# Kernel tuning notes

Measured on AMD Instinct MI355X. Metric: run time of the kernel, lower is better.

## Reference

```python
import jax, jax.numpy as jnp
import numpy as np

N_NODES = 50000
N_EDGES = 800000
IN_F = 128
OUT_F = 128
EDGE_F = 6


def setup_inputs() -> dict:
    key = jax.random.key(0)
    k1, k2, k3, k4, k5, k6, k7 = jax.random.split(key, 7)
    nodeFeatures = jax.random.normal(k1, (N_NODES, IN_F), dtype=jnp.float32)
    edgeIndex = jax.random.randint(k2, (N_EDGES, 2), 0, N_NODES, dtype=jnp.int64)
    edgeFeatures = jax.random.normal(k3, (N_EDGES, EDGE_F), dtype=jnp.float32)
    # nn.Linear params (kaiming-uniform-ish init scale)
    lim_n = 1.0 / np.sqrt(IN_F)
    lim_e = 1.0 / np.sqrt(EDGE_F)
    W = jax.random.uniform(k4, (IN_F, OUT_F), minval=-lim_n, maxval=lim_n, dtype=jnp.float32)
    b = jax.random.uniform(k5, (OUT_F,), minval=-lim_n, maxval=lim_n, dtype=jnp.float32)
    We = jax.random.uniform(k6, (EDGE_F, OUT_F), minval=-lim_e, maxval=lim_e, dtype=jnp.float32)
    be = jax.random.uniform(k7, (OUT_F,), minval=-lim_e, maxval=lim_e, dtype=jnp.float32)
    return {"nodeFeatures": nodeFeatures, "edgeIndex": edgeIndex,
            "edgeFeatures": edgeFeatures, "W": W, "b": b, "We": We, "be": be}


def reference(nodeFeatures, edgeIndex, edgeFeatures, W, b, We, be):
    # node linear: [N, out]
    transformed = nodeFeatures @ W + b
    # edge linear: [E, out]
    edgeMsg = edgeFeatures @ We + be
    src = edgeIndex[:, 0]
    dst = edgeIndex[:, 1]
    # per-edge message = transformed[src] + edgeMsg, scatter-add into dst
    messages = transformed[src] + edgeMsg  # [E, out]
    aggregated = jax.ops.segment_sum(messages, dst, num_segments=nodeFeatures.shape[0])
    return jax.nn.relu(aggregated)
```

## Files before the change

### kernel.cpp

```cpp
#include <hip/hip_runtime.h>
#include <hip/hip_bf16.h>
#include <stdint.h>

#define IN_F 128
#define EDGE_F 6

using bf16x8 = __attribute__((ext_vector_type(8))) short;
using f32x4  = __attribute__((ext_vector_type(4))) float;

__device__ __forceinline__ float bf2f(unsigned short u) {
    return __uint_as_float(((unsigned int)u) << 16);
}
__device__ __forceinline__ unsigned short f2bfbits(float f) {
    __hip_bfloat16 h = __float2bfloat16(f);
    return *reinterpret_cast<unsigned short*>(&h);
}
__device__ __forceinline__ unsigned int packbf(float a, float b) {
    return ((unsigned int)f2bfbits(b) << 16) | (unsigned int)f2bfbits(a);
}

__global__ __launch_bounds__(256) void hist_cast(
        const int* __restrict__ eidx, const float* __restrict__ ef,
        int* __restrict__ cnt, int* __restrict__ rank,
        uint4* __restrict__ efp, int n_edges,
        const float* __restrict__ nf, unsigned short* __restrict__ nfb,
        int n_cast) {
    const int t = blockIdx.x * 256 + threadIdx.x;
    if (t < n_edges) {
        const int2 pr = reinterpret_cast<const int2*>(eidx)[t];
        const float2* efs = reinterpret_cast<const float2*>(ef + (size_t)t * EDGE_F);
        const float2 f0 = efs[0], f1 = efs[1], f2 = efs[2];
        uint4 q;
        q.x = (unsigned int)pr.x;
        q.y = packbf(f0.x, f0.y);
        q.z = packbf(f1.x, f1.y);
        q.w = packbf(f2.x, f2.y);
        efp[t] = q;
        rank[t] = atomicAdd(&cnt[pr.y], 1);
    }
    const int stride = gridDim.x * 256;
    for (int i = t; i < n_cast; i += stride) {
        const float4 lo = reinterpret_cast<const float4*>(nf)[2 * i];
        const float4 hi = reinterpret_cast<const float4*>(nf)[2 * i + 1];
        uint4 o;
        o.x = packbf(lo.x, lo.y); o.y = packbf(lo.z, lo.w);
        o.z = packbf(hi.x, hi.y); o.w = packbf(hi.z, hi.w);
        reinterpret_cast<uint4*>(nfb)[i] = o;
    }
}

__global__ __launch_bounds__(256) void scan_fused(
        const int* __restrict__ cnt, int* __restrict__ rowptr, int n, int nblk,
        unsigned long long* __restrict__ agg,
        const float* __restrict__ W, const float* __restrict__ b,
        const float* __restrict__ We, const float* __restrict__ be,
        unsigned short* __restrict__ Wpack, float* __restrict__ W2pack) {
    const int tid = threadIdx.x;
    const int blk = blockIdx.x;
    if (blk == nblk) {
        for (int idx = tid; idx < 16384; idx += 256) {
            int j = idx & 7, lane = (idx >> 3) & 63, ft = (idx >> 9) & 7, kb = idx >> 12;
            int k = kb * 32 + (lane >> 4) * 8 + j;
            int f = ft * 16 + (lane & 15);
            Wpack[idx] = f2bfbits(W[k * 128 + f]);
        }
        for (int idx = tid; idx < 1024; idx += 256) {
            int j = idx >> 7, f = idx & 127;
            float w = 0.f;
            if (j < 6)       w = We[j * 128 + f];
            else if (j == 6) w = b[f] + be[f];
            W2pack[idx] = w;
        }
        return;
    }
    __shared__ int sh[256];
    const int idx = blk * 256 + tid;
    const int v = (idx < n) ? cnt[idx] : 0;
    sh[tid] = v;
    __syncthreads();
    for (int off = 1; off < 256; off <<= 1) {
        int t2 = (tid >= off) ? sh[tid - off] : 0;
        __syncthreads();
        sh[tid] += t2;
        __syncthreads();
    }
    const int incl = sh[tid];
    if (tid == 0)
        atomicExch(&agg[blk], (1ULL << 32) | (unsigned int)sh[255]);
    int pre = 0;
    if (tid < blk) {
        unsigned long long x;
        do { x = atomicAdd(&agg[tid], 0ULL); } while ((x >> 32) == 0);
        pre = (int)(unsigned int)x;
    }
    __syncthreads();
    sh[tid] = pre;
    __syncthreads();
    for (int off = 128; off > 0; off >>= 1) {
        if (tid < off) sh[tid] += sh[tid + off];
        __syncthreads();
    }
    const int off0 = sh[0];
    if (idx < n) rowptr[idx] = off0 + incl - v;
    if (blk == nblk - 1 && tid == 255) rowptr[n] = off0 + incl;
}

__global__ __launch_bounds__(256) void fill_csr(
        const int* __restrict__ eidx, const int* __restrict__ rowptr,
        const int* __restrict__ rank, const uint4* __restrict__ efp,
        uint4* __restrict__ rec, int n_edges) {
    int e = blockIdx.x * 256 + threadIdx.x;
    if (e >= n_edges) return;
    const int dst = reinterpret_cast<const int2*>(eidx)[e].y;
    const int pos = rowptr[dst] + rank[e];
    rec[pos] = efp[e];
}

__global__ __launch_bounds__(256) void aggregate_bf16(
        const unsigned short* __restrict__ nfb, const uint4* __restrict__ rec,
        const int* __restrict__ rowptr, unsigned short* __restrict__ S,
        unsigned short* __restrict__ E8, int n_nodes) {
    const int lane = threadIdx.x & 63;
    const int wv = __builtin_amdgcn_readfirstlane(threadIdx.x >> 6);
    const int n = blockIdx.x * 4 + wv;
    if (n >= n_nodes) return;
    const int r0 = rowptr[n], r1 = rowptr[n + 1];
    const int deg = r1 - r0;
    float ax = 0.f, ay = 0.f;
    float e0 = 0.f, e1 = 0.f, e2 = 0.f, e3 = 0.f, e4 = 0.f, e5 = 0.f;
    int i = r0;
    for (; i + 7 < r1; i += 8) {
        uint4 q[8];
        unsigned int u[8];
#pragma unroll
        for (int j = 0; j < 8; ++j) q[j] = rec[i + j];
#pragma unroll
        for (int j = 0; j < 8; ++j)
            u[j] = reinterpret_cast<const unsigned int*>(nfb + (size_t)(int)q[j].x * IN_F)[lane];
#pragma unroll
        for (int j = 0; j < 8; ++j) {
            ax += bf2f((unsigned short)u[j]);
            ay += bf2f((unsigned short)(u[j] >> 16));
            e0 += bf2f((unsigned short)q[j].y);
            e1 += bf2f((unsigned short)(q[j].y >> 16));
            e2 += bf2f((unsigned short)q[j].z);
            e3 += bf2f((unsigned short)(q[j].z >> 16));
            e4 += bf2f((unsigned short)q[j].w);
            e5 += bf2f((unsigned short)(q[j].w >> 16));
        }
    }
    for (; i + 3 < r1; i += 4) {
        uint4 q[4];
        unsigned int u[4];
#pragma unroll
        for (int j = 0; j < 4; ++j) q[j] = rec[i + j];
#pragma unroll
        for (int j = 0; j < 4; ++j)
            u[j] = reinterpret_cast<const unsigned int*>(nfb + (size_t)(int)q[j].x * IN_F)[lane];
#pragma unroll
        for (int j = 0; j < 4; ++j) {
            ax += bf2f((unsigned short)u[j]);
            ay += bf2f((unsigned short)(u[j] >> 16));
            e0 += bf2f((unsigned short)q[j].y);
            e1 += bf2f((unsigned short)(q[j].y >> 16));
            e2 += bf2f((unsigned short)q[j].z);
            e3 += bf2f((unsigned short)(q[j].z >> 16));
            e4 += bf2f((unsigned short)q[j].w);
            e5 += bf2f((unsigned short)(q[j].w >> 16));
        }
    }
    for (; i < r1; ++i) {
        const uint4 q0 = rec[i];
        const unsigned int u0 = reinterpret_cast<const unsigned int*>(nfb + (size_t)(int)q0.x * IN_F)[lane];
        ax += bf2f((unsigned short)u0); ay += bf2f((unsigned short)(u0 >> 16));
        e0 += bf2f((unsigned short)q0.y); e1 += bf2f((unsigned short)(q0.y >> 16));
        e2 += bf2f((unsigned short)q0.z); e3 += bf2f((unsigned short)(q0.z >> 16));
        e4 += bf2f((unsigned short)q0.w); e5 += bf2f((unsigned short)(q0.w >> 16));
    }
    unsigned short* row = S + (size_t)n * IN_F;
    reinterpret_cast<unsigned int*>(row)[lane] = packbf(ax, ay);
    if (lane == 0) {
        uint4 q;
        q.x = packbf(e0, e1);
        q.y = packbf(e2, e3);
        q.z = packbf(e4, e5);
        q.w = packbf((float)deg, 0.f);
        *reinterpret_cast<uint4*>(E8 + (size_t)n * 8) = q;
    }
}

__global__ __launch_bounds__(256) void gemm_mfma(
        const unsigned short* __restrict__ S, const unsigned short* __restrict__ E8,
        const unsigned short* __restrict__ Wpack, const float* __restrict__ W2pack,
        float* __restrict__ out, int n_nodes) {
    __shared__ __align__(16) short Wl[16384];
    __shared__ float W2l[1024];
    const int tid = threadIdx.x;
    for (int i = tid; i < 2048; i += 256)
        reinterpret_cast<uint4*>(Wl)[i] = reinterpret_cast<const uint4*>(Wpack)[i];
    for (int i = tid; i < 1024; i += 256) W2l[i] = W2pack[i];

    const int wv = tid >> 6, lane = tid & 63;
    const int m = lane & 15, quad = lane >> 4;
    const int n0 = blockIdx.x * 64 + wv * 16;

    const int arow = min(n0 + m, n_nodes - 1);
    const unsigned short* ap = S + (size_t)arow * IN_F + quad * 8;
    bf16x8 a[4];
#pragma unroll
    for (int kb = 0; kb < 4; ++kb)
        a[kb] = *reinterpret_cast<const bf16x8*>(ap + kb * 32);

    __syncthreads();

    f32x4 acc[8];
#pragma unroll
    for (int ft = 0; ft < 8; ++ft) acc[ft] = (f32x4){0.f, 0.f, 0.f, 0.f};

#pragma unroll
    for (int kb = 0; kb < 4; ++kb) {
#pragma unroll
        for (int ft = 0; ft < 8; ++ft) {
            const bf16x8 bfrag =
                reinterpret_cast<const bf16x8*>(Wl)[(kb * 8 + ft) * 64 + lane];
            acc[ft] = __builtin_amdgcn_mfma_f32_16x16x32_bf16(a[kb], bfrag, acc[ft], 0, 0, 0);
        }
    }

    float e[4][7];
#pragma unroll
    for (int r = 0; r < 4; ++r) {
        const int n = min(n0 + quad * 4 + r, n_nodes - 1);
        const uint4 q = *reinterpret_cast<const uint4*>(E8 + (size_t)n * 8);
        e[r][0] = bf2f((unsigned short)q.x); e[r][1] = bf2f((unsigned short)(q.x >> 16));
        e[r][2] = bf2f((unsigned short)q.y); e[r][3] = bf2f((unsigned short)(q.y >> 16));
        e[r][4] = bf2f((unsigned short)q.z); e[r][5] = bf2f((unsigned short)(q.z >> 16));
        e[r][6] = bf2f((unsigned short)q.w);
    }
#pragma unroll
    for (int ft = 0; ft < 8; ++ft) {
        const int f = ft * 16 + m;
        float w2[7];
#pragma unroll
        for (int j = 0; j < 7; ++j) w2[j] = W2l[j * 128 + f];
#pragma unroll
        for (int r = 0; r < 4; ++r) {
            const int n = n0 + quad * 4 + r;
            if (n < n_nodes) {
                float v = acc[ft][r];
#pragma unroll
                for (int j = 0; j < 7; ++j) v += e[r][j] * w2[j];
                out[(size_t)n * 128 + f] = fmaxf(v, 0.f);
            }
        }
    }
}

extern "C" void kernel_launch(void* const* d_in, const int* in_sizes, int n_in,
                              void* d_out, int out_size, void* d_ws, size_t ws_size,
                              hipStream_t stream) {
    const float* nf = (const float*)d_in[0];
    const int* eidx = (const int*)d_in[1];
    const float* ef = (const float*)d_in[2];
    const float* W  = (const float*)d_in[3];
    const float* b  = (const float*)d_in[4];
    const float* We = (const float*)d_in[5];
    const float* be = (const float*)d_in[6];
    float* out = (float*)d_out;

    const int n_nodes = in_sizes[0] / IN_F;
    const int n_edges = in_sizes[1] / 2;

    uint4* rec = (uint4*)d_ws;
    uint4* efp = rec + n_edges;
    unsigned short* S = (unsigned short*)(efp + n_edges);
    unsigned short* E8 = S + (size_t)n_nodes * IN_F;
    unsigned short* Wpack = E8 + (size_t)n_nodes * 8;
    float* W2pack = (float*)(Wpack + 16384);
    int* cnt = (int*)(W2pack + 1024);
    unsigned long long* agg = (unsigned long long*)(cnt + n_nodes);
    int* rowptr = (int*)(agg + 256);
    int* rank   = rowptr + n_nodes + 1;
    unsigned short* nfb = (unsigned short*)(rank + n_edges);

    hipMemsetAsync(cnt, 0, (size_t)n_nodes * 4 + 256 * 8, stream);

    const int eb = (n_edges + 255) / 256;
    const int nblk = (n_nodes + 255) / 256;
    const int n_cast = n_nodes * (IN_F / 8);

    hist_cast<<<eb, 256, 0, stream>>>(eidx, ef, cnt, rank, efp, n_edges, nf, nfb, n_cast);
    scan_fused<<<nblk + 1, 256, 0, stream>>>(cnt, rowptr, n_nodes, nblk, agg,
                                             W, b, We, be, Wpack, W2pack);
    fill_csr<<<eb, 256, 0, stream>>>(eidx, rowptr, rank, efp, rec, n_edges);

    aggregate_bf16<<<(n_nodes + 3) / 4, 256, 0, stream>>>(nfb, rec, rowptr, S, E8, n_nodes);
    gemm_mfma<<<(n_nodes + 63) / 64, 256, 0, stream>>>(S, E8, Wpack, W2pack, out, n_nodes);
}
```

Before: 206.8 us.

## Fuse neighbor aggregation and MFMA GEMM into one kernel via LDS staging

Merges the aggregation kernel and the GEMM kernel. Each 256-thread block aggregates 64 destination rows into padded shared memory, then runs the MFMA projection straight from LDS. W fragments are read from global/L2 instead of being staged in shared memory. This removes the S/E8 global round trip and one kernel launch. In exchange, only 782 blocks remain, each wave serially gathers 16 rows, and the MFMA phase waits on the slowest row, so latency hiding and load balance may get worse.

```diff
diff --git a/kernel.cpp b/kernel.cpp
--- a/kernel.cpp
+++ b/kernel.cpp
@@ -4,6 +4,8 @@
 
 #define IN_F 128
 #define EDGE_F 6
+#define ROWS 64
+#define RSTRIDE 136
 
 using bf16x8 = __attribute__((ext_vector_type(8))) short;
 using f32x4  = __attribute__((ext_vector_type(4))) float;
@@ -116,103 +118,97 @@
     rec[pos] = efp[e];
 }
 
-__global__ __launch_bounds__(256) void aggregate_bf16(
+__global__ __launch_bounds__(256) void agg_gemm(
         const unsigned short* __restrict__ nfb, const uint4* __restrict__ rec,
-        const int* __restrict__ rowptr, unsigned short* __restrict__ S,
-        unsigned short* __restrict__ E8, int n_nodes) {
-    const int lane = threadIdx.x & 63;
-    const int wv = __builtin_amdgcn_readfirstlane(threadIdx.x >> 6);
-    const int n = blockIdx.x * 4 + wv;
-    if (n >= n_nodes) return;
-    const int r0 = rowptr[n], r1 = rowptr[n + 1];
-    const int deg = r1 - r0;
-    float ax = 0.f, ay = 0.f;
-    float e0 = 0.f, e1 = 0.f, e2 = 0.f, e3 = 0.f, e4 = 0.f, e5 = 0.f;
-    int i = r0;
-    for (; i + 7 < r1; i += 8) {
-        uint4 q[8];
-        unsigned int u[8];
-#pragma unroll
-        for (int j = 0; j < 8; ++j) q[j] = rec[i + j];
-#pragma unroll
-        for (int j = 0; j < 8; ++j)
-            u[j] = reinterpret_cast<const unsigned int*>(nfb + (size_t)(int)q[j].x * IN_F)[lane];
-#pragma unroll
-        for (int j = 0; j < 8; ++j) {
-            ax += bf2f((unsigned short)u[j]);
-            ay += bf2f((unsigned short)(u[j] >> 16));
-            e0 += bf2f((unsigned short)q[j].y);
-            e1 += bf2f((unsigned short)(q[j].y >> 16));
-            e2 += bf2f((unsigned short)q[j].z);
-            e3 += bf2f((unsigned short)(q[j].z >> 16));
-            e4 += bf2f((unsigned short)q[j].w);
-            e5 += bf2f((unsigned short)(q[j].w >> 16));
-        }
-    }
-    for (; i + 3 < r1; i += 4) {
-        uint4 q[4];
-        unsigned int u[4];
-#pragma unroll
-        for (int j = 0; j < 4; ++j) q[j] = rec[i + j];
-#pragma unroll
-        for (int j = 0; j < 4; ++j)
-            u[j] = reinterpret_cast<const unsigned int*>(nfb + (size_t)(int)q[j].x * IN_F)[lane];
-#pragma unroll
-        for (int j = 0; j < 4; ++j) {
-            ax += bf2f((unsigned short)u[j]);
-            ay += bf2f((unsigned short)(u[j] >> 16));
-            e0 += bf2f((unsigned short)q[j].y);
-            e1 += bf2f((unsigned short)(q[j].y >> 16));
-            e2 += bf2f((unsigned short)q[j].z);
-            e3 += bf2f((unsigned short)(q[j].z >> 16));
-            e4 += bf2f((unsigned short)q[j].w);
-            e5 += bf2f((unsigned short)(q[j].w >> 16));
-        }
-    }
-    for (; i < r1; ++i) {
-        const uint4 q0 = rec[i];
-        const unsigned int u0 = reinterpret_cast<const unsigned int*>(nfb + (size_t)(int)q0.x * IN_F)[lane];
-        ax += bf2f((unsigned short)u0); ay += bf2f((unsigned short)(u0 >> 16));
-        e0 += bf2f((unsigned short)q0.y); e1 += bf2f((unsigned short)(q0.y >> 16));
-        e2 += bf2f((unsigned short)q0.z); e3 += bf2f((unsigned short)(q0.z >> 16));
-        e4 += bf2f((unsigned short)q0.w); e5 += bf2f((unsigned short)(q0.w >> 16));
-    }
-    unsigned short* row = S + (size_t)n * IN_F;
-    reinterpret_cast<unsigned int*>(row)[lane] = packbf(ax, ay);
-    if (lane == 0) {
-        uint4 q;
-        q.x = packbf(e0, e1);
-        q.y = packbf(e2, e3);
-        q.z = packbf(e4, e5);
-        q.w = packbf((float)deg, 0.f);
-        *reinterpret_cast<uint4*>(E8 + (size_t)n * 8) = q;
-    }
-}
-
-__global__ __launch_bounds__(256) void gemm_mfma(
-        const unsigned short* __restrict__ S, const unsigned short* __restrict__ E8,
+        const int* __restrict__ rowptr,
         const unsigned short* __restrict__ Wpack, const float* __restrict__ W2pack,
         float* __restrict__ out, int n_nodes) {
-    __shared__ __align__(16) short Wl[16384];
-    __shared__ float W2l[1024];
+    __shared__ __align__(16) unsigned short Sl[ROWS * RSTRIDE];
+    __shared__ __align__(16) unsigned short E8l[ROWS * 8];
     const int tid = threadIdx.x;
-    for (int i = tid; i < 2048; i += 256)
-        reinterpret_cast<uint4*>(Wl)[i] = reinterpret_cast<const uint4*>(Wpack)[i];
-    for (int i = tid; i < 1024; i += 256) W2l[i] = W2pack[i];
-
-    const int wv = tid >> 6, lane = tid & 63;
+    const int lane = tid & 63;
+    const int wv = tid >> 6;
+    const int nb0 = blockIdx.x * ROWS;
+
+    for (int r = wv; r < ROWS; r += 4) {
+        const int n = nb0 + r;
+        float ax = 0.f, ay = 0.f;
+        float e0 = 0.f, e1 = 0.f, e2 = 0.f, e3 = 0.f, e4 = 0.f, e5 = 0.f;
+        int deg = 0;
+        if (n < n_nodes) {
+            const int r0 = rowptr[n], r1 = rowptr[n + 1];
+            deg = r1 - r0;
+            int i = r0;
+            for (; i + 7 < r1; i += 8) {
+                uint4 q[8];
+                unsigned int u[8];
+#pragma unroll
+                for (int j = 0; j < 8; ++j) q[j] = rec[i + j];
+#pragma unroll
+                for (int j = 0; j < 8; ++j)
+                    u[j] = reinterpret_cast<const unsigned int*>(nfb + (size_t)(int)q[j].x * IN_F)[lane];
+#pragma unroll
+                for (int j = 0; j < 8; ++j) {
+                    ax += bf2f((unsigned short)u[j]);
+                    ay += bf2f((unsigned short)(u[j] >> 16));
+                    e0 += bf2f((unsigned short)q[j].y);
+                    e1 += bf2f((unsigned short)(q[j].y >> 16));
+                    e2 += bf2f((unsigned short)q[j].z);
+                    e3 += bf2f((unsigned short)(q[j].z >> 16));
+                    e4 += bf2f((unsigned short)q[j].w);
+                    e5 += bf2f((unsigned short)(q[j].w >> 16));
+                }
+            }
+            for (; i + 3 < r1; i += 4) {
+                uint4 q[4];
+                unsigned int u[4];
+#pragma unroll
+                for (int j = 0; j < 4; ++j) q[j] = rec[i + j];
+#pragma unroll
+                for (int j = 0; j < 4; ++j)
+                    u[j] = reinterpret_cast<const unsigned int*>(nfb + (size_t)(int)q[j].x * IN_F)[lane];
+#pragma unroll
+                for (int j = 0; j < 4; ++j) {
+                    ax += bf2f((unsigned short)u[j]);
+                    ay += bf2f((unsigned short)(u[j] >> 16));
+                    e0 += bf2f((unsigned short)q[j].y);
+                    e1 += bf2f((unsigned short)(q[j].y >> 16));
+                    e2 += bf2f((unsigned short)q[j].z);
+                    e3 += bf2f((unsigned short)(q[j].z >> 16));
+                    e4 += bf2f((unsigned short)q[j].w);
+                    e5 += bf2f((unsigned short)(q[j].w >> 16));
+                }
+            }
+            for (; i < r1; ++i) {
+                const uint4 q0 = rec[i];
+                const unsigned int u0 = reinterpret_cast<const unsigned int*>(nfb + (size_t)(int)q0.x * IN_F)[lane];
+                ax += bf2f((unsigned short)u0); ay += bf2f((unsigned short)(u0 >> 16));
+                e0 += bf2f((unsigned short)q0.y); e1 += bf2f((unsigned short)(q0.y >> 16));
+                e2 += bf2f((unsigned short)q0.z); e3 += bf2f((unsigned short)(q0.z >> 16));
+                e4 += bf2f((unsigned short)q0.w); e5 += bf2f((unsigned short)(q0.w >> 16));
+            }
+        }
+        reinterpret_cast<unsigned int*>(Sl + r * RSTRIDE)[lane] = packbf(ax, ay);
+        if (lane == 0) {
+            uint4 q;
+            q.x = packbf(e0, e1);
+            q.y = packbf(e2, e3);
+            q.z = packbf(e4, e5);
+            q.w = packbf((float)deg, 0.f);
+            *reinterpret_cast<uint4*>(E8l + r * 8) = q;
+        }
+    }
+    __syncthreads();
+
     const int m = lane & 15, quad = lane >> 4;
-    const int n0 = blockIdx.x * 64 + wv * 16;
-
-    const int arow = min(n0 + m, n_nodes - 1);
-    const unsigned short* ap = S + (size_t)arow * IN_F + quad * 8;
+    const int rbase = wv * 16;
+
+    const unsigned short* ap = Sl + (rbase + m) * RSTRIDE + quad * 8;
     bf16x8 a[4];
 #pragma unroll
     for (int kb = 0; kb < 4; ++kb)
         a[kb] = *reinterpret_cast<const bf16x8*>(ap + kb * 32);
 
-    __syncthreads();
-
     f32x4 acc[8];
 #pragma unroll
     for (int ft = 0; ft < 8; ++ft) acc[ft] = (f32x4){0.f, 0.f, 0.f, 0.f};
@@ -222,7 +218,7 @@
 #pragma unroll
         for (int ft = 0; ft < 8; ++ft) {
             const bf16x8 bfrag =
-                reinterpret_cast<const bf16x8*>(Wl)[(kb * 8 + ft) * 64 + lane];
+                reinterpret_cast<const bf16x8*>(Wpack)[(kb * 8 + ft) * 64 + lane];
             acc[ft] = __builtin_amdgcn_mfma_f32_16x16x32_bf16(a[kb], bfrag, acc[ft], 0, 0, 0);
         }
     }
@@ -230,8 +226,8 @@
     float e[4][7];
 #pragma unroll
     for (int r = 0; r < 4; ++r) {
-        const int n = min(n0 + quad * 4 + r, n_nodes - 1);
-        const uint4 q = *reinterpret_cast<const uint4*>(E8 + (size_t)n * 8);
+        const int rl = rbase + quad * 4 + r;
+        const uint4 q = *reinterpret_cast<const uint4*>(E8l + rl * 8);
         e[r][0] = bf2f((unsigned short)q.x); e[r][1] = bf2f((unsigned short)(q.x >> 16));
         e[r][2] = bf2f((unsigned short)q.y); e[r][3] = bf2f((unsigned short)(q.y >> 16));
         e[r][4] = bf2f((unsigned short)q.z); e[r][5] = bf2f((unsigned short)(q.z >> 16));
@@ -242,10 +238,10 @@
         const int f = ft * 16 + m;
         float w2[7];
 #pragma unroll
-        for (int j = 0; j < 7; ++j) w2[j] = W2l[j * 128 + f];
+        for (int j = 0; j < 7; ++j) w2[j] = W2pack[j * 128 + f];
 #pragma unroll
         for (int r = 0; r < 4; ++r) {
-            const int n = n0 + quad * 4 + r;
+            const int n = nb0 + rbase + quad * 4 + r;
             if (n < n_nodes) {
                 float v = acc[ft][r];
 #pragma unroll
@@ -273,9 +269,7 @@
 
     uint4* rec = (uint4*)d_ws;
     uint4* efp = rec + n_edges;
-    unsigned short* S = (unsigned short*)(efp + n_edges);
-    unsigned short* E8 = S + (size_t)n_nodes * IN_F;
-    unsigned short* Wpack = E8 + (size_t)n_nodes * 8;
+    unsigned short* Wpack = (unsigned short*)(efp + n_edges);
     float* W2pack = (float*)(Wpack + 16384);
     int* cnt = (int*)(W2pack + 1024);
     unsigned long long* agg = (unsigned long long*)(cnt + n_nodes);
@@ -294,6 +288,6 @@
                                              W, b, We, be, Wpack, W2pack);
     fill_csr<<<eb, 256, 0, stream>>>(eidx, rowptr, rank, efp, rec, n_edges);
 
-    aggregate_bf16<<<(n_nodes + 3) / 4, 256, 0, stream>>>(nfb, rec, rowptr, S, E8, n_nodes);
-    gemm_mfma<<<(n_nodes + 63) / 64, 256, 0, stream>>>(S, E8, Wpack, W2pack, out, n_nodes);
-}
+    agg_gemm<<<(n_nodes + ROWS - 1) / ROWS, 256, 0, stream>>>(
+        nfb, rec, rowptr, Wpack, W2pack, out, n_nodes);
+}
```

After: 268.4 us. 1.3x slower.
